# Kernel optimization log

Hardware: AMD Instinct MI355X
Metric: run time of the kernel (lower is better)

## Reference

```python
import jax, jax.numpy as jnp
import numpy as np

N = 500_000      # evaluation points
M = 8            # Nmode
K = 4            # Clebsch branches
NPSI = 256       # psi grid points
X0 = 0.0
H = 1.0 / (NPSI - 1)


def _cubic_interp(f, x):
    """Cubic Hermite spline (C1, FD slopes) on a uniform psi grid, extrapolating.
    f: [NPSI, C] table, x: [N] query points -> [N, C]."""
    u = (x - X0) / H
    i = jnp.clip(jnp.floor(u).astype(jnp.int32), 0, NPSI - 2)
    s = (u - i.astype(x.dtype))[:, None]           # local coord, may be outside [0,1] (extrap)
    d = jnp.gradient(f, axis=0) / H                # FD derivatives [NPSI, C]
    f0, f1, d0, d1 = f[i], f[i + 1], d[i], d[i + 1]
    s2 = s * s
    s3 = s2 * s
    return ((2 * s3 - 3 * s2 + 1) * f0 + (s3 - 2 * s2 + s) * H * d0
            + (-2 * s3 + 3 * s2) * f1 + (s3 - s2) * H * d1)


def setup_inputs() -> dict:
    key = jax.random.key(0)
    ks = jax.random.split(key, 12)
    pg = jnp.linspace(0.0, 1.0, NPSI, dtype=jnp.float32)
    inp = {
        "t": jnp.float32(0.5),
        "psi": jax.random.uniform(ks[0], (N,), jnp.float32, 0.05, 0.95),
        "theta": jax.random.uniform(ks[1], (N,), jnp.float32, -jnp.pi, jnp.pi),
        "varphi": jax.random.uniform(ks[2], (N,), jnp.float32, 0.0, 2 * jnp.pi),
        # smooth Clebsch profiles on the psi grid (safety factor q and alpha offset)
        "q_vals": (1.0 + 2.5 * pg ** 2).astype(jnp.float32),
        "aoff_vals": (0.3 * jnp.sin(2 * jnp.pi * pg)).astype(jnp.float32),
        "theta0": jax.random.uniform(ks[3], (M,), jnp.float32, -jnp.pi, jnp.pi),
        "omega": jax.random.uniform(ks[4], (M,), jnp.float32, 0.5, 2.0),
        "psi0": jax.random.uniform(ks[5], (M,), jnp.float32, 0.2, 0.8),
        "psi_scale": jax.random.uniform(ks[6], (M,), jnp.float32, 0.05, 0.15),
        "alpha_scale": jax.random.uniform(ks[7], (M,), jnp.float32, 0.2, 0.6),
        "gh_coefs": 0.5 * jax.random.normal(ks[8], (M, 4, 6), jnp.float32),
        "n": jax.random.randint(ks[9], (M,), 1, 12, jnp.int32),
    }
    return inp


def reference(t, psi, theta, varphi, q_vals, aoff_vals, theta0, omega, psi0,
              psi_scale, alpha_scale, gh_coefs, n):
    # Clebsch mapping: alpha_k(psi, theta) = q(psi) * (theta + 2*pi*k) + alpha_off(psi)
    qa = _cubic_interp(jnp.stack([q_vals, aoff_vals], axis=-1), psi)  # [N,2]
    q, aoff = qa[:, 0], qa[:, 1]
    kk = 2 * jnp.pi * jnp.arange(K, dtype=psi.dtype)
    alpha = q[:, None] * (theta[:, None] + kk[None, :]) + aoff[:, None]    # [N,K]
    # alpha0(psi; mode) table built from the Clebsch profiles (mirrors __init__)
    alpha0_grid = q_vals[:, None] * theta0[None, :] + aoff_vals[:, None]   # [NPSI,M]
    alpha0 = _cubic_interp(alpha0_grid, psi)                               # [N,M]

    x = (psi[:, None] - psi0) / psi_scale                                  # [N,M]
    y = (alpha[:, None, :] - alpha0[:, :, None]) / alpha_scale[None, :, None]  # [N,M,K]
    g = jnp.exp(-0.5 * (x[:, :, None] ** 2 + y ** 2))                      # [N,M,K]

    c = gh_coefs  # [M,4,6]
    h10 = x[:, :, None, None]
    h01 = y[:, :, :, None]
    h20 = (4 * x ** 2 - 2)[:, :, None, None]
    h11 = (x[:, :, None] * y)[:, :, :, None]
    h02 = (4 * y ** 2 - 2)[:, :, :, None]
    p = (c[None, :, None, :, 0] + c[None, :, None, :, 1] * h10
         + c[None, :, None, :, 2] * h01 + c[None, :, None, :, 3] * h20
         + c[None, :, None, :, 4] * h11 + c[None, :, None, :, 5] * h02)    # [N,M,K,4]
    p = p * g[:, :, :, None]

    nf = n.astype(psi.dtype)
    # alpha - alpha0 == y * alpha_scale
    phase = omega[None, :, None] * t - nf[None, :, None] * (
        varphi[:, None, None] - y * alpha_scale[None, :, None])            # [N,M,K]
    cp, sp = jnp.cos(phase), jnp.sin(phase)
    phi = jnp.sum(p[..., 0] * cp - p[..., 1] * sp, axis=(1, 2))            # [N]
    apar = jnp.sum(p[..., 2] * cp - p[..., 3] * sp, axis=(1, 2))           # [N]
    return phi, apar
```

## Files before the change

### kernel.cpp

```cpp
#include <hip/hip_runtime.h>

#define NPSI 256
#define MM 8
#define KK 4
#define NMP (MM / 2)
#define TBF (NMP * 60)

typedef float v2f __attribute__((ext_vector_type(2)));

#if __has_builtin(__builtin_amdgcn_exp2f)
#define EXP2F(x) __builtin_amdgcn_exp2f(x)
#else
#define EXP2F(x) exp2f(x)
#endif
#define SIN_REV(x) __builtin_amdgcn_sinf(x)
#define COS_REV(x) __builtin_amdgcn_cosf(x)

#define VFMA(a,b,c) __builtin_elementwise_fma((v2f)(a),(v2f)(b),(v2f)(c))

__device__ inline float cubic_q(const float* __restrict__ q_vals, float psi) {
    float u = psi * (float)(NPSI - 1);
    int   i = (int)floorf(u);
    i = min(max(i, 0), NPSI - 2);
    float s  = u - (float)i;
    float f0 = q_vals[i];
    float f1 = q_vals[i + 1];
    float d0 = (i == 0)        ? (f1 - f0) : 0.5f * (f1 - q_vals[i - 1]);
    float d1 = (i == NPSI - 2) ? (f1 - f0) : 0.5f * (q_vals[i + 2] - f0);
    float s2 = s * s, s3 = s2 * s;
    return (2.f * s3 - 3.f * s2 + 1.f) * f0
         + (s3 - 2.f * s2 + s)         * d0
         + (-2.f * s3 + 3.f * s2)      * f1
         + (s3 - s2)                   * d1;
}

__global__ __launch_bounds__(64) void prep_kernel(
    const float* __restrict__ theta0_a,
    const float* __restrict__ omega_a,
    const float* __restrict__ psi0_a,
    const float* __restrict__ psi_scale_a,
    const float* __restrict__ alpha_scale_a,
    const float* __restrict__ gh_a,
    const int*   __restrict__ n_a,
    float* __restrict__ tb)
{
    const int tid = threadIdx.x;
    if (tid < MM) {
        const int m = tid, mp = m >> 1, lane = m & 1;
        float* b = tb + mp * 60 + lane;
        const float invps = 1.0f / psi_scale_a[m];
        b[0]  = psi0_a[m] * invps;
        b[2]  = invps;
        b[4]  = 1.0f / alpha_scale_a[m];
        b[6]  = (float)n_a[m];
        b[8]  = theta0_a[m];
        b[10] = omega_a[m];
    }
    if (tid < MM * 4) {
        const int m = tid >> 2, comp = tid & 3;
        const int mp = m >> 1, lane = m & 1;
        const float* c = gh_a + m * 24 + comp * 6;
        float* b = tb + mp * 60 + (6 + comp * 6) * 2 + lane;
        b[0]  = fmaf(-2.f, c[3] + c[5], c[0]);
        b[2]  = c[1];
        b[4]  = c[3];
        b[6]  = c[2];
        b[8]  = c[4];
        b[10] = c[5];
    }
}

__global__ __launch_bounds__(256, 4) void eik_kernel(
    const float* __restrict__ t_ptr,
    const float* __restrict__ psi_a,
    const float* __restrict__ theta_a,
    const float* __restrict__ varphi_a,
    const float* __restrict__ q_vals,
    const float* __restrict__ tb,
    float* __restrict__ out,
    int N)
{
    const int gid = blockIdx.x * blockDim.x + threadIdx.x;
    if (gid >= N) return;

    const float INV2PI = 0.15915494309189533577f;
    const float TWO_PI = 6.28318530717958647692f;
    const float NEXPC  = -0.72134752044448170368f;

    const float t     = t_ptr[0];
    const float psi   = psi_a[gid];
    const float theta = theta_a[gid];
    const float vp    = varphi_a[gid] * INV2PI;

    const float q    = cubic_q(q_vals, psi);
    const float q2pi = q * TWO_PI;
    const float tt   = t * INV2PI;

    v2f phi = (v2f)0.f, apar = (v2f)0.f;

    #pragma unroll 1
    for (int mp = 0; mp < NMP; ++mp) {
        const v2f* T = (const v2f*)tb + mp * 30;
        const v2f psi0ps = T[0], invps = T[1], invas = T[2];
        const v2f nf = T[3], th0 = T[4], om = T[5];

        const v2f x  = VFMA((v2f)psi, invps, -psi0ps);
        const v2f x2 = x * x;
        const v2f x4 = 4.f * x2;

        v2f pa[4], pb[4], pf[4];
        #pragma unroll
        for (int comp = 0; comp < 4; ++comp) {
            const v2f* B = T + 6 + comp * 6;
            pa[comp] = VFMA(B[2], x4, VFMA(B[1], x, B[0]));
            pb[comp] = VFMA(B[4], x, B[3]);
            pf[comp] = B[5];
        }

        const v2f dth  = (v2f)theta - th0;
        const v2f qdth = q * dth;
        const v2f y0   = qdth * invas;
        const v2f dy   = q2pi * invas;
        const v2f dphr = nf * q;
        const v2f p0r  = VFMA(nf, qdth * INV2PI,
                              VFMA(om, (v2f)tt, -nf * vp));

        v2f cp, sp, cd, sd;
        cp.x = COS_REV(p0r.x);  cp.y = COS_REV(p0r.y);
        sp.x = SIN_REV(p0r.x);  sp.y = SIN_REV(p0r.y);
        cd.x = COS_REV(dphr.x); cd.y = COS_REV(dphr.y);
        sd.x = SIN_REV(dphr.x); sd.y = SIN_REV(dphr.y);

        v2f t2v[KK], gv[KK];
        {
            v2f yk = y0;
            #pragma unroll
            for (int k = 0; k < KK; ++k) {
                const v2f t2 = VFMA(yk, yk, x2);
                t2v[k] = t2;
                const v2f ta = t2 * NEXPC;
                gv[k].x = EXP2F(ta.x);
                gv[k].y = EXP2F(ta.y);
                yk = yk + dy;
            }
        }

        v2f y = y0;
        #pragma unroll
        for (int k = 0; k < KK; ++k) {
            const v2f y4 = VFMA((v2f)4.f, t2v[k], -x4);
            const v2f gc = gv[k] * cp;
            const v2f gs = gv[k] * sp;
            const v2f p0 = VFMA(pf[0], y4, VFMA(pb[0], y, pa[0]));
            const v2f p1 = VFMA(pf[1], y4, VFMA(pb[1], y, pa[1]));
            const v2f p2 = VFMA(pf[2], y4, VFMA(pb[2], y, pa[2]));
            const v2f p3 = VFMA(pf[3], y4, VFMA(pb[3], y, pa[3]));
            phi  = VFMA(p0, gc, phi);
            phi  = VFMA(-p1, gs, phi);
            apar = VFMA(p2, gc, apar);
            apar = VFMA(-p3, gs, apar);
            if (k < KK - 1) {
                const v2f ncp = VFMA(cp, cd, -(sp * sd));
                const v2f nsp = VFMA(sp, cd,  cp * sd);
                cp = ncp; sp = nsp;
                y = y + dy;
            }
        }
    }

    out[gid]     = phi.x + phi.y;
    out[N + gid] = apar.x + apar.y;
}

extern "C" void kernel_launch(void* const* d_in, const int* in_sizes, int n_in,
                              void* d_out, int out_size, void* d_ws, size_t ws_size,
                              hipStream_t stream) {
    const float* t       = (const float*)d_in[0];
    const float* psi     = (const float*)d_in[1];
    const float* theta   = (const float*)d_in[2];
    const float* varphi  = (const float*)d_in[3];
    const float* q_vals  = (const float*)d_in[4];
    const float* theta0  = (const float*)d_in[6];
    const float* omega   = (const float*)d_in[7];
    const float* psi0    = (const float*)d_in[8];
    const float* psc     = (const float*)d_in[9];
    const float* asc     = (const float*)d_in[10];
    const float* gh      = (const float*)d_in[11];
    const int*   n_arr   = (const int*)d_in[12];

    const int N = in_sizes[1];
    float* out = (float*)d_out;
    float* tb  = (float*)d_ws;

    prep_kernel<<<1, 64, 0, stream>>>(theta0, omega, psi0, psc, asc,
                                      gh, n_arr, tb);

    const int block = 256;
    const int grid  = (N + block - 1) / block;
    eik_kernel<<<grid, block, 0, stream>>>(t, psi, theta, varphi, q_vals,
                                           tb, out, N);
}
```

Before: 93.02 us.

## Precompute q spline polynomial table, simplify y^2 term, unroll mode loop

The prep kernel now precomputes per-interval cubic polynomial coefficients for q as one float4 per interval, so each thread does a single vector load and a Horner evaluation instead of four scattered loads plus Hermite basis arithmetic. The c5 coefficient is pre-scaled by 4, so the y^2 term is computed directly from y*y without storing t2 per branch, which lowers register pressure. The mode-pair loop is unrolled by 2 and the occupancy hint is raised from 4 to 5 blocks. The unroll and the higher occupancy target pull against each other on registers and could cause spills.

```diff
diff --git a/kernel.cpp b/kernel.cpp
--- a/kernel.cpp
+++ b/kernel.cpp
@@ -4,9 +4,9 @@
 #define MM 8
 #define KK 4
 #define NMP (MM / 2)
-#define TBF (NMP * 60)
 
 typedef float v2f __attribute__((ext_vector_type(2)));
+typedef float v4f __attribute__((ext_vector_type(4)));
 
 #if __has_builtin(__builtin_amdgcn_exp2f)
 #define EXP2F(x) __builtin_amdgcn_exp2f(x)
@@ -18,23 +18,8 @@
 
 #define VFMA(a,b,c) __builtin_elementwise_fma((v2f)(a),(v2f)(b),(v2f)(c))
 
-__device__ inline float cubic_q(const float* __restrict__ q_vals, float psi) {
-    float u = psi * (float)(NPSI - 1);
-    int   i = (int)floorf(u);
-    i = min(max(i, 0), NPSI - 2);
-    float s  = u - (float)i;
-    float f0 = q_vals[i];
-    float f1 = q_vals[i + 1];
-    float d0 = (i == 0)        ? (f1 - f0) : 0.5f * (f1 - q_vals[i - 1]);
-    float d1 = (i == NPSI - 2) ? (f1 - f0) : 0.5f * (q_vals[i + 2] - f0);
-    float s2 = s * s, s3 = s2 * s;
-    return (2.f * s3 - 3.f * s2 + 1.f) * f0
-         + (s3 - 2.f * s2 + s)         * d0
-         + (-2.f * s3 + 3.f * s2)      * f1
-         + (s3 - s2)                   * d1;
-}
-
-__global__ __launch_bounds__(64) void prep_kernel(
+__global__ __launch_bounds__(256) void prep_kernel(
+    const float* __restrict__ q_vals,
     const float* __restrict__ theta0_a,
     const float* __restrict__ omega_a,
     const float* __restrict__ psi0_a,
@@ -45,6 +30,18 @@
     float* __restrict__ tb)
 {
     const int tid = threadIdx.x;
+    if (tid < NPSI - 1) {
+        const int i = tid;
+        const float f0 = q_vals[i], f1 = q_vals[i + 1];
+        const float d0 = (i == 0)        ? (f1 - f0) : 0.5f * (f1 - q_vals[i - 1]);
+        const float d1 = (i == NPSI - 2) ? (f1 - f0) : 0.5f * (q_vals[i + 2] - f0);
+        v4f c;
+        c.x = f0;
+        c.y = d0;
+        c.z = 3.f * (f1 - f0) - 2.f * d0 - d1;
+        c.w = 2.f * (f0 - f1) + d0 + d1;
+        *(v4f*)(tb + 256 + 4 * i) = c;
+    }
     if (tid < MM) {
         const int m = tid, mp = m >> 1, lane = m & 1;
         float* b = tb + mp * 60 + lane;
@@ -66,16 +63,15 @@
         b[4]  = c[3];
         b[6]  = c[2];
         b[8]  = c[4];
-        b[10] = c[5];
+        b[10] = 4.f * c[5];
     }
 }
 
-__global__ __launch_bounds__(256, 4) void eik_kernel(
+__global__ __launch_bounds__(256, 5) void eik_kernel(
     const float* __restrict__ t_ptr,
     const float* __restrict__ psi_a,
     const float* __restrict__ theta_a,
     const float* __restrict__ varphi_a,
-    const float* __restrict__ q_vals,
     const float* __restrict__ tb,
     float* __restrict__ out,
     int N)
@@ -92,13 +88,21 @@
     const float theta = theta_a[gid];
     const float vp    = varphi_a[gid] * INV2PI;
 
-    const float q    = cubic_q(q_vals, psi);
+    float q;
+    {
+        const float u = psi * (float)(NPSI - 1);
+        int i = (int)floorf(u);
+        i = min(max(i, 0), NPSI - 2);
+        const float s = u - (float)i;
+        const v4f cq = *(const v4f*)(tb + 256 + 4 * i);
+        q = fmaf(s, fmaf(s, fmaf(s, cq.w, cq.z), cq.y), cq.x);
+    }
     const float q2pi = q * TWO_PI;
     const float tt   = t * INV2PI;
 
     v2f phi = (v2f)0.f, apar = (v2f)0.f;
 
-    #pragma unroll 1
+    #pragma unroll 2
     for (int mp = 0; mp < NMP; ++mp) {
         const v2f* T = (const v2f*)tb + mp * 30;
         const v2f psi0ps = T[0], invps = T[1], invas = T[2];
@@ -108,13 +112,13 @@
         const v2f x2 = x * x;
         const v2f x4 = 4.f * x2;
 
-        v2f pa[4], pb[4], pf[4];
+        v2f pa[4], pb[4], pf4[4];
         #pragma unroll
         for (int comp = 0; comp < 4; ++comp) {
             const v2f* B = T + 6 + comp * 6;
-            pa[comp] = VFMA(B[2], x4, VFMA(B[1], x, B[0]));
-            pb[comp] = VFMA(B[4], x, B[3]);
-            pf[comp] = B[5];
+            pa[comp]  = VFMA(B[2], x4, VFMA(B[1], x, B[0]));
+            pb[comp]  = VFMA(B[4], x, B[3]);
+            pf4[comp] = B[5];
         }
 
         const v2f dth  = (v2f)theta - th0;
@@ -131,13 +135,12 @@
         cd.x = COS_REV(dphr.x); cd.y = COS_REV(dphr.y);
         sd.x = SIN_REV(dphr.x); sd.y = SIN_REV(dphr.y);
 
-        v2f t2v[KK], gv[KK];
+        v2f gv[KK];
         {
             v2f yk = y0;
             #pragma unroll
             for (int k = 0; k < KK; ++k) {
                 const v2f t2 = VFMA(yk, yk, x2);
-                t2v[k] = t2;
                 const v2f ta = t2 * NEXPC;
                 gv[k].x = EXP2F(ta.x);
                 gv[k].y = EXP2F(ta.y);
@@ -148,13 +151,13 @@
         v2f y = y0;
         #pragma unroll
         for (int k = 0; k < KK; ++k) {
-            const v2f y4 = VFMA((v2f)4.f, t2v[k], -x4);
+            const v2f y2 = y * y;
             const v2f gc = gv[k] * cp;
             const v2f gs = gv[k] * sp;
-            const v2f p0 = VFMA(pf[0], y4, VFMA(pb[0], y, pa[0]));
-            const v2f p1 = VFMA(pf[1], y4, VFMA(pb[1], y, pa[1]));
-            const v2f p2 = VFMA(pf[2], y4, VFMA(pb[2], y, pa[2]));
-            const v2f p3 = VFMA(pf[3], y4, VFMA(pb[3], y, pa[3]));
+            const v2f p0 = VFMA(pf4[0], y2, VFMA(pb[0], y, pa[0]));
+            const v2f p1 = VFMA(pf4[1], y2, VFMA(pb[1], y, pa[1]));
+            const v2f p2 = VFMA(pf4[2], y2, VFMA(pb[2], y, pa[2]));
+            const v2f p3 = VFMA(pf4[3], y2, VFMA(pb[3], y, pa[3]));
             phi  = VFMA(p0, gc, phi);
             phi  = VFMA(-p1, gs, phi);
             apar = VFMA(p2, gc, apar);
@@ -192,11 +195,11 @@
     float* out = (float*)d_out;
     float* tb  = (float*)d_ws;
 
-    prep_kernel<<<1, 64, 0, stream>>>(theta0, omega, psi0, psc, asc,
-                                      gh, n_arr, tb);
+    prep_kernel<<<1, 256, 0, stream>>>(q_vals, theta0, omega, psi0, psc, asc,
+                                       gh, n_arr, tb);
 
     const int block = 256;
     const int grid  = (N + block - 1) / block;
-    eik_kernel<<<grid, block, 0, stream>>>(t, psi, theta, varphi, q_vals,
+    eik_kernel<<<grid, block, 0, stream>>>(t, psi, theta, varphi,
                                            tb, out, N);
 }
```

After: 93.25 us. About the same (+0.2%).
